# Optimization experiments

Measured on AMD Instinct MI355X. Metric: run time of the kernel, lower is better.

The kernel has to match this reference:

```python
import jax, jax.numpy as jnp
import numpy as np

DIM = 16
HID = 32

def setup_inputs() -> dict:
    key = jax.random.key(0)
    ks = jax.random.split(key, 5)
    B, S = 32768, 64
    x = jax.random.normal(ks[0], (B, S, DIM), dtype=jnp.float32)
    # LayerNorm params (torch defaults: weight=1, bias=0)
    ln_w = jnp.ones((DIM,), dtype=jnp.float32)
    ln_b = jnp.zeros((DIM,), dtype=jnp.float32)
    # Linear params, torch-style init scale ~ 1/sqrt(fan_in)
    w1 = jax.random.uniform(ks[1], (HID, DIM), jnp.float32, -1.0, 1.0) / np.sqrt(DIM)
    b1 = jax.random.uniform(ks[2], (HID,), jnp.float32, -1.0, 1.0) / np.sqrt(DIM)
    w2 = jax.random.uniform(ks[3], (DIM, HID), jnp.float32, -1.0, 1.0) / np.sqrt(HID)
    b2 = jax.random.uniform(ks[4], (DIM,), jnp.float32, -1.0, 1.0) / np.sqrt(HID)
    return {"x": x, "ln_w": ln_w, "ln_b": ln_b, "w1": w1, "b1": b1, "w2": w2, "b2": b2}

def _layernorm(x, w, b, eps=1e-5):
    mu = jnp.mean(x, axis=-1, keepdims=True)
    var = jnp.mean(jnp.square(x - mu), axis=-1, keepdims=True)
    return (x - mu) * jax.lax.rsqrt(var + eps) * w + b

def reference(x, ln_w, ln_b, w1, b1, w2, b2):
    h = _layernorm(x, ln_w, ln_b)
    h = jnp.einsum('bsd,hd->bsh', h, w1) + b1
    h = jax.nn.gelu(h, approximate=False)  # torch nn.GELU default is exact erf
    h = jnp.einsum('bsh,dh->bsd', h, w2) + b2
    return x + h
```

## Files before the change

kernel.cpp:

```cpp
#include <hip/hip_runtime.h>
#include <math.h>

#define DIM 16
#define HID 32

__global__ __launch_bounds__(256) void fused_ln_mlp_kernel(
    const float* __restrict__ x,
    const float* __restrict__ ln_w,
    const float* __restrict__ ln_b,
    const float* __restrict__ w1,
    const float* __restrict__ b1,
    const float* __restrict__ w2,
    const float* __restrict__ b2,
    float* __restrict__ out,
    int nrows)
{
    int row = blockIdx.x * blockDim.x + threadIdx.x;
    if (row >= nrows) return;

    const float* xr = x + (size_t)row * DIM;

    float xv[DIM];
    {
        float4 t0 = *(const float4*)(xr + 0);
        float4 t1 = *(const float4*)(xr + 4);
        float4 t2 = *(const float4*)(xr + 8);
        float4 t3 = *(const float4*)(xr + 12);
        xv[0] = t0.x; xv[1] = t0.y; xv[2]  = t0.z; xv[3]  = t0.w;
        xv[4] = t1.x; xv[5] = t1.y; xv[6]  = t1.z; xv[7]  = t1.w;
        xv[8] = t2.x; xv[9] = t2.y; xv[10] = t2.z; xv[11] = t2.w;
        xv[12] = t3.x; xv[13] = t3.y; xv[14] = t3.z; xv[15] = t3.w;
    }

    float mu = 0.0f;
    #pragma unroll
    for (int i = 0; i < DIM; i++) mu += xv[i];
    mu *= (1.0f / DIM);

    float var = 0.0f;
    #pragma unroll
    for (int i = 0; i < DIM; i++) {
        float d = xv[i] - mu;
        var += d * d;
    }
    var *= (1.0f / DIM);
    float rstd = rsqrtf(var + 1e-5f);

    float a = rstd;
    float c = -mu * rstd;
    float xn[DIM];
    #pragma unroll
    for (int i = 0; i < DIM; i++) {
        float xhat = fmaf(xv[i], a, c);
        xn[i] = fmaf(xhat, ln_w[i], ln_b[i]);
    }

    float g[HID];
    #pragma unroll
    for (int h = 0; h < HID; h++) {
        float acc = b1[h];
        #pragma unroll
        for (int d = 0; d < DIM; d++) acc = fmaf(xn[d], w1[h * DIM + d], acc);
        g[h] = 0.5f * acc * (1.0f + erff(acc * 0.70710678118654752f));
    }

    #pragma unroll
    for (int d = 0; d < DIM; d++) {
        float acc = b2[d];
        #pragma unroll
        for (int h = 0; h < HID; h++) acc = fmaf(g[h], w2[d * HID + h], acc);
        xv[d] += acc;
    }

    float* outr = out + (size_t)row * DIM;
    *(float4*)(outr + 0)  = make_float4(xv[0],  xv[1],  xv[2],  xv[3]);
    *(float4*)(outr + 4)  = make_float4(xv[4],  xv[5],  xv[6],  xv[7]);
    *(float4*)(outr + 8)  = make_float4(xv[8],  xv[9],  xv[10], xv[11]);
    *(float4*)(outr + 12) = make_float4(xv[12], xv[13], xv[14], xv[15]);
}

extern "C" void kernel_launch(void* const* d_in, const int* in_sizes, int n_in,
                              void* d_out, int out_size, void* d_ws, size_t ws_size,
                              hipStream_t stream) {
    const float* x    = (const float*)d_in[0];
    const float* ln_w = (const float*)d_in[1];
    const float* ln_b = (const float*)d_in[2];
    const float* w1   = (const float*)d_in[3];
    const float* b1   = (const float*)d_in[4];
    const float* w2   = (const float*)d_in[5];
    const float* b2   = (const float*)d_in[6];
    float* out = (float*)d_out;

    int nrows = in_sizes[0] / DIM;
    int block = 256;
    int grid = (nrows + block - 1) / block;

    fused_ln_mlp_kernel<<<grid, block, 0, stream>>>(
        x, ln_w, ln_b, w1, b1, w2, b2, out, nrows);
}
```

Measured before the change: 290.6 us.

## Use packed FP32 FMAs and polynomial erf approximation for GELU

Rewrites the LayerNorm and both matmul loops to use two-wide float vectors so the compiler can emit packed FP32 FMA instructions (v_pk_fma_f32) on CDNA. Replaces the library erff with the Abramowitz-Stegun polynomial approximation, built on hardware reciprocal and fast exp, to cut transcendental cost. The approximation has roughly 1e-7 absolute error, which may slightly change numerical output. The kernel is compute-heavy per row, so reducing ALU instruction count is the target.

```diff
diff --git a/kernel.cpp b/kernel.cpp
--- a/kernel.cpp
+++ b/kernel.cpp
@@ -3,6 +3,24 @@
 
 #define DIM 16
 #define HID 32
+
+typedef float v2f __attribute__((ext_vector_type(2)));
+
+__device__ inline float gelu_erf(float x) {
+    const float kInvSqrt2 = 0.70710678118654752f;
+    float z  = x * kInvSqrt2;
+    float az = fabsf(z);
+    float t  = __builtin_amdgcn_rcpf(fmaf(0.3275911f, az, 1.0f));
+    float e  = __expf(-az * az);
+    float p  = fmaf(t, 1.061405429f, -1.453152027f);
+    p = fmaf(t, p, 1.421413741f);
+    p = fmaf(t, p, -0.284496736f);
+    p = fmaf(t, p, 0.254829592f);
+    p = p * t;
+    float erf_abs = fmaf(-p, e, 1.0f);
+    float erfv = copysignf(erf_abs, z);
+    return 0.5f * x * (1.0f + erfv);
+}
 
 __global__ __launch_bounds__(256) void fused_ln_mlp_kernel(
     const float* __restrict__ x,
@@ -20,63 +38,77 @@
 
     const float* xr = x + (size_t)row * DIM;
 
-    float xv[DIM];
+    v2f xv2[8];
     {
         float4 t0 = *(const float4*)(xr + 0);
         float4 t1 = *(const float4*)(xr + 4);
         float4 t2 = *(const float4*)(xr + 8);
         float4 t3 = *(const float4*)(xr + 12);
-        xv[0] = t0.x; xv[1] = t0.y; xv[2]  = t0.z; xv[3]  = t0.w;
-        xv[4] = t1.x; xv[5] = t1.y; xv[6]  = t1.z; xv[7]  = t1.w;
-        xv[8] = t2.x; xv[9] = t2.y; xv[10] = t2.z; xv[11] = t2.w;
-        xv[12] = t3.x; xv[13] = t3.y; xv[14] = t3.z; xv[15] = t3.w;
+        xv2[0] = (v2f){t0.x, t0.y}; xv2[1] = (v2f){t0.z, t0.w};
+        xv2[2] = (v2f){t1.x, t1.y}; xv2[3] = (v2f){t1.z, t1.w};
+        xv2[4] = (v2f){t2.x, t2.y}; xv2[5] = (v2f){t2.z, t2.w};
+        xv2[6] = (v2f){t3.x, t3.y}; xv2[7] = (v2f){t3.z, t3.w};
     }
 
-    float mu = 0.0f;
+    v2f s = xv2[0] + xv2[1];
+    s += xv2[2] + xv2[3];
+    s += xv2[4] + xv2[5];
+    s += xv2[6] + xv2[7];
+    float mu = (s.x + s.y) * (1.0f / DIM);
+
+    v2f mu2 = (v2f){mu, mu};
+    v2f vs = (v2f){0.0f, 0.0f};
     #pragma unroll
-    for (int i = 0; i < DIM; i++) mu += xv[i];
-    mu *= (1.0f / DIM);
+    for (int i = 0; i < 8; i++) {
+        v2f d = xv2[i] - mu2;
+        vs = __builtin_elementwise_fma(d, d, vs);
+    }
+    float var = (vs.x + vs.y) * (1.0f / DIM);
+    float a = __builtin_amdgcn_rsqf(var + 1e-5f);
+    float c = -mu * a;
 
-    float var = 0.0f;
+    const v2f* lnw2 = (const v2f*)ln_w;
+    const v2f* lnb2 = (const v2f*)ln_b;
+    v2f a2 = (v2f){a, a};
+    v2f c2 = (v2f){c, c};
+    v2f xn2[8];
     #pragma unroll
-    for (int i = 0; i < DIM; i++) {
-        float d = xv[i] - mu;
-        var += d * d;
-    }
-    var *= (1.0f / DIM);
-    float rstd = rsqrtf(var + 1e-5f);
-
-    float a = rstd;
-    float c = -mu * rstd;
-    float xn[DIM];
-    #pragma unroll
-    for (int i = 0; i < DIM; i++) {
-        float xhat = fmaf(xv[i], a, c);
-        xn[i] = fmaf(xhat, ln_w[i], ln_b[i]);
+    for (int i = 0; i < 8; i++) {
+        v2f xhat = __builtin_elementwise_fma(xv2[i], a2, c2);
+        xn2[i] = __builtin_elementwise_fma(xhat, lnw2[i], lnb2[i]);
     }
 
     float g[HID];
     #pragma unroll
     for (int h = 0; h < HID; h++) {
-        float acc = b1[h];
+        const v2f* wr = (const v2f*)(w1 + h * DIM);
+        v2f acc = (v2f){0.0f, 0.0f};
         #pragma unroll
-        for (int d = 0; d < DIM; d++) acc = fmaf(xn[d], w1[h * DIM + d], acc);
-        g[h] = 0.5f * acc * (1.0f + erff(acc * 0.70710678118654752f));
+        for (int j = 0; j < 8; j++) acc = __builtin_elementwise_fma(xn2[j], wr[j], acc);
+        float hv = acc.x + acc.y + b1[h];
+        g[h] = gelu_erf(hv);
     }
 
+    v2f g2[HID / 2];
+    #pragma unroll
+    for (int k = 0; k < HID / 2; k++) g2[k] = (v2f){g[2 * k], g[2 * k + 1]};
+
+    float yv[DIM];
     #pragma unroll
     for (int d = 0; d < DIM; d++) {
-        float acc = b2[d];
+        const v2f* wr = (const v2f*)(w2 + d * HID);
+        v2f acc = (v2f){0.0f, 0.0f};
         #pragma unroll
-        for (int h = 0; h < HID; h++) acc = fmaf(g[h], w2[d * HID + h], acc);
-        xv[d] += acc;
+        for (int k = 0; k < HID / 2; k++) acc = __builtin_elementwise_fma(g2[k], wr[k], acc);
+        float xval = (d & 1) ? xv2[d >> 1].y : xv2[d >> 1].x;
+        yv[d] = acc.x + acc.y + b2[d] + xval;
     }
 
     float* outr = out + (size_t)row * DIM;
-    *(float4*)(outr + 0)  = make_float4(xv[0],  xv[1],  xv[2],  xv[3]);
-    *(float4*)(outr + 4)  = make_float4(xv[4],  xv[5],  xv[6],  xv[7]);
-    *(float4*)(outr + 8)  = make_float4(xv[8],  xv[9],  xv[10], xv[11]);
-    *(float4*)(outr + 12) = make_float4(xv[12], xv[13], xv[14], xv[15]);
+    *(float4*)(outr + 0)  = make_float4(yv[0],  yv[1],  yv[2],  yv[3]);
+    *(float4*)(outr + 4)  = make_float4(yv[4],  yv[5],  yv[6],  yv[7]);
+    *(float4*)(outr + 8)  = make_float4(yv[8],  yv[9],  yv[10], yv[11]);
+    *(float4*)(outr + 12) = make_float4(yv[12], yv[13], yv[14], yv[15]);
 }
 
 extern "C" void kernel_launch(void* const* d_in, const int* in_sizes, int n_in,
```

Result: faster. 258.3 us (-11.1%).
